# Kernel optimization log

Measured on AMD Instinct MI355X. Metric: run time of the kernel, lower is better.

Reference implementation:

```python
import jax, jax.numpy as jnp
import numpy as np

V, E, H, DV = 32000, 512, 1024, 512
B, K = 64, 49


def setup_inputs():
    key = jax.random.key(0)
    ks = jax.random.split(key, 16)
    p = lambda i, shape: jax.random.normal(ks[i], shape, dtype=jnp.float32) * 0.02
    return {
        "thought": jax.random.normal(ks[0], (B, H), dtype=jnp.float32),
        "visual_features": jax.random.normal(ks[1], (B, K, DV), dtype=jnp.float32),
        "max_len": 64,
        "embedding": p(2, (V, E)),
        "Wih1": p(3, (4 * H, E)), "Whh1": p(4, (4 * H, H)),
        "bih1": jnp.zeros((4 * H,), jnp.float32), "bhh1": jnp.zeros((4 * H,), jnp.float32),
        "Wih2": p(5, (4 * H, H)), "Whh2": p(6, (4 * H, H)),
        "bih2": jnp.zeros((4 * H,), jnp.float32), "bhh2": jnp.zeros((4 * H,), jnp.float32),
        "Wg1": p(7, (H, H)), "bg1": jnp.zeros((H,), jnp.float32),
        "Wg2": p(8, (1, H)), "bg2": jnp.zeros((1,), jnp.float32),
        "Wo": p(9, (V, H)), "bo": jnp.zeros((V,), jnp.float32),
        "Wv": p(10, (H, DV)), "bv": jnp.zeros((H,), jnp.float32),
        "ln_g": jnp.ones((H,), jnp.float32), "ln_b": jnp.zeros((H,), jnp.float32),
    }


def _lstm_cell(x, h, c, Wih, Whh, bih, bhh):
    # PyTorch LSTM gate order: i, f, g, o
    z = x @ Wih.T + h @ Whh.T + bih + bhh
    i, f, g, o = jnp.split(z, 4, axis=-1)
    c_new = jax.nn.sigmoid(f) * c + jax.nn.sigmoid(i) * jnp.tanh(g)
    h_new = jax.nn.sigmoid(o) * jnp.tanh(c_new)
    return h_new, c_new


def reference(thought, visual_features, max_len, embedding, Wih1, Whh1, bih1, bhh1,
              Wih2, Whh2, bih2, bbh2=None, bih2_dummy=None, **_unused):
    raise RuntimeError('placeholder')


def reference(thought, visual_features, max_len, embedding, Wih1, Whh1, bih1, bhh1,
              Wih2, Whh2, bih2, bhh2, Wg1, bg1, Wg2, bg2, Wo, bo, Wv, bv, ln_g, ln_b):
    Bsz, Hd = thought.shape
    temperature = 0.4  # epoch = 0 -> 0.4 + 0.4*0
    top_p = 0.7        # epoch = 0 -> 0.7 + 0.2*0
    scale = 1.0 / jnp.sqrt(jnp.asarray(Hd, jnp.float32))
    # visual_proj: Linear + LayerNorm (Dropout is identity in eval mode)
    vp = visual_features @ Wv.T + bv
    mu = vp.mean(-1, keepdims=True)
    var = vp.var(-1, keepdims=True)
    vp = (vp - mu) / jnp.sqrt(var + 1e-5) * ln_g + ln_b  # [B,K,H]
    b_idx = jnp.arange(Bsz)
    # carry: (h1,c1,h2,c2, input token, last-3 token history, history validity)
    init = (thought, jnp.zeros_like(thought), thought, jnp.zeros_like(thought),
            jnp.full((Bsz,), 1, jnp.int32),
            jnp.zeros((Bsz, 3), jnp.int32), jnp.zeros((Bsz, 3), jnp.bool_))
    keys = jax.random.split(jax.random.key(42), max_len)

    def step(carry, key):
        h1, c1, h2, c2, inp, hist, histv = carry
        emb = embedding[inp]  # [B,E]
        h1, c1 = _lstm_cell(emb, h1, c1, Wih1, Whh1, bih1, bhh1)
        h2, c2 = _lstm_cell(h1, h2, c2, Wih2, Whh2, bih2, bhh2)
        gate = jax.nn.sigmoid(jnp.tanh(h2 @ Wg1.T + bg1) @ Wg2.T + bg2)  # [B,1]
        out = h2 * gate
        attn = jax.nn.softmax(jnp.einsum('bh,bkh->bk', out, vp) * scale, axis=-1)
        out = out + jnp.einsum('bk,bkh->bh', attn, vp)
        logits = out @ Wo.T + bo  # [B,V]
        # repetition penalty: -2.0 once per UNIQUE token in last-3 history (set semantics via .max)
        pen = jnp.zeros_like(logits).at[b_idx[:, None], hist].max(histv.astype(logits.dtype))
        logits = (logits - 2.0 * pen) / temperature
        # nucleus (top-p) filtering, matching top_k_top_p_filtering with top_k=0
        order = jnp.argsort(-logits, axis=-1)
        sl = jnp.take_along_axis(logits, order, axis=-1)
        cum = jnp.cumsum(jax.nn.softmax(sl, axis=-1), axis=-1)
        rem = cum > top_p
        rem = jnp.concatenate([jnp.zeros_like(rem[:, :1]), rem[:, :-1]], axis=-1)
        mask = jnp.zeros_like(rem).at[b_idx[:, None], order].set(rem)
        logits = jnp.where(mask, -jnp.inf, logits)
        nxt = jax.random.categorical(key, logits).astype(jnp.int32)  # multinomial sample
        hist = jnp.concatenate([hist[:, 1:], nxt[:, None]], axis=1)
        histv = jnp.concatenate([histv[:, 1:], jnp.ones((Bsz, 1), jnp.bool_)], axis=1)
        return (h1, c1, h2, c2, nxt, hist, histv), nxt

    _, toks = jax.lax.scan(step, init, keys)
    return toks.T  # [B, max_len]
```

## Files before the change

### kernel.cpp

```cpp
#include <hip/hip_runtime.h>
#include <hip/hip_bf16.h>
#include <stdint.h>


#define B_   64
#define H_   1024
#define E_   512
#define DV_  512
#define KV_  49
#define V_   32000
#define T_   64

__device__ __forceinline__ uint32_t rotl32(uint32_t x, int r) {
  return (x << r) | (x >> (32 - r));
}
__device__ __forceinline__ void tf2x32(uint32_t k0, uint32_t k1,
                                       uint32_t x0, uint32_t x1,
                                       uint32_t& o0, uint32_t& o1) {
  uint32_t ks0 = k0, ks1 = k1, ks2 = k0 ^ k1 ^ 0x1BD11BDAu;
  x0 += ks0; x1 += ks1;
#define RND_(r) { x0 += x1; x1 = rotl32(x1, r) ^ x0; }
  RND_(13) RND_(15) RND_(26) RND_(6)  x0 += ks1; x1 += ks2 + 1u;
  RND_(17) RND_(29) RND_(16) RND_(24) x0 += ks2; x1 += ks0 + 2u;
  RND_(13) RND_(15) RND_(26) RND_(6)  x0 += ks0; x1 += ks1 + 3u;
  RND_(17) RND_(29) RND_(16) RND_(24) x0 += ks1; x1 += ks2 + 4u;
  RND_(13) RND_(15) RND_(26) RND_(6)  x0 += ks2; x1 += ks0 + 5u;
#undef RND_
  o0 = x0; o1 = x1;
}

__device__ __forceinline__ unsigned key_of(float f) {
  unsigned u = __float_as_uint(f);
  return (u & 0x80000000u) ? ~u : (u | 0x80000000u);
}
__device__ __forceinline__ float sigf(float x) { return 1.0f / (1.0f + expf(-x)); }

__global__ __launch_bounds__(256)
void gemm32(const float* __restrict__ A0, int lda0, const float* __restrict__ W0,
            int ldw0, int K0, float* __restrict__ out0, int ldo0, int nt0,
            const float* __restrict__ A1, int lda1, const float* __restrict__ W1,
            int ldw1, int K1, float* __restrict__ out1, int ldo1) {
  __shared__ __align__(16) float As[64][36];
  __shared__ __align__(16) float Ws[32][36];
  int tid = threadIdx.x;
  int bx = blockIdx.x;
  const float* A; const float* W; float* out;
  int lda, ldw, K, ldo, n0;
  if (bx < nt0) { A = A0; W = W0; out = out0; lda = lda0; ldw = ldw0; K = K0; ldo = ldo0; n0 = bx * 32; }
  else          { A = A1; W = W1; out = out1; lda = lda1; ldw = ldw1; K = K1; ldo = ldo1; n0 = (bx - nt0) * 32; }
  int m0 = blockIdx.y * 64;
  int tc = tid & 15, tr = tid >> 4;
  float acc[4][2] = {};
  for (int kc = 0; kc < K; kc += 32) {
#pragma unroll
    for (int l = tid; l < 768; l += 256) {
      if (l < 512) {
        int r = l >> 3, c4 = l & 7;
        *(float4*)&As[r][c4 * 4] =
            *(const float4*)&A[(long long)(m0 + r) * lda + kc + c4 * 4];
      } else {
        int q = l - 512;
        int r = q >> 3, c4 = q & 7;
        *(float4*)&Ws[r][c4 * 4] =
            *(const float4*)&W[(long long)(n0 + r) * ldw + kc + c4 * 4];
      }
    }
    __syncthreads();
#pragma unroll
    for (int kk4 = 0; kk4 < 8; kk4++) {
      float4 a4[4], w4[2];
#pragma unroll
      for (int i = 0; i < 4; i++) a4[i] = *(const float4*)&As[tr * 4 + i][kk4 * 4];
#pragma unroll
      for (int j = 0; j < 2; j++) w4[j] = *(const float4*)&Ws[tc * 2 + j][kk4 * 4];
#pragma unroll
      for (int i = 0; i < 4; i++)
#pragma unroll
        for (int j = 0; j < 2; j++) {
          acc[i][j] = fmaf(a4[i].x, w4[j].x, acc[i][j]);
          acc[i][j] = fmaf(a4[i].y, w4[j].y, acc[i][j]);
          acc[i][j] = fmaf(a4[i].z, w4[j].z, acc[i][j]);
          acc[i][j] = fmaf(a4[i].w, w4[j].w, acc[i][j]);
        }
    }
    __syncthreads();
  }
#pragma unroll
  for (int i = 0; i < 4; i++)
#pragma unroll
    for (int j = 0; j < 2; j++)
      out[(long long)(m0 + tr * 4 + i) * ldo + n0 + tc * 2 + j] = acc[i][j];
}

__global__ __launch_bounds__(256)
void ln_vp(float* __restrict__ vp, const float* __restrict__ bv,
           const float* __restrict__ g, const float* __restrict__ bt) {
  int row = blockIdx.x, tid = threadIdx.x;
  __shared__ float buf[H_];
  __shared__ float red[256];
  float* p = vp + (long long)row * H_;
  for (int h = tid; h < H_; h += 256) buf[h] = __fadd_rn(p[h], bv[h]);
  __syncthreads();
  float s = 0;
  for (int h = tid; h < H_; h += 256) s += buf[h];
  red[tid] = s; __syncthreads();
  for (int off = 128; off > 0; off >>= 1) { if (tid < off) red[tid] += red[tid + off]; __syncthreads(); }
  float mu = red[0] / (float)H_;
  __syncthreads();
  float vs = 0;
  for (int h = tid; h < H_; h += 256) { float d = buf[h] - mu; vs += d * d; }
  red[tid] = vs; __syncthreads();
  for (int off = 128; off > 0; off >>= 1) { if (tid < off) red[tid] += red[tid + off]; __syncthreads(); }
  float var = red[0] / (float)H_;
  float sq = sqrtf(var + 1e-5f);
  for (int h = tid; h < H_; h += 256) {
    float nrm = __fdiv_rn(__fsub_rn(buf[h], mu), sq);
    p[h] = __fadd_rn(__fmul_rn(nrm, g[h]), bt[h]);
  }
}

__global__ __launch_bounds__(256)
void lstm_cell2(const float* __restrict__ dx, const float* __restrict__ dh,
                const float* __restrict__ bih, const float* __restrict__ bhh,
                float* __restrict__ c,
                float* __restrict__ hA, int ldA, float* __restrict__ hB, int ldB) {
  int idx = blockIdx.x * 256 + threadIdx.x;
  int b = idx >> 10, h = idx & 1023;
  float z[4];
#pragma unroll
  for (int g = 0; g < 4; g++) {
    int j = g * 1024 + h;
    float s = __fadd_rn(dx[b * 4096 + j], dh[b * 4096 + j]);
    s = __fadd_rn(s, bih[j]);
    s = __fadd_rn(s, bhh[j]);
    z[g] = s;
  }
  float fc = __fmul_rn(sigf(z[1]), c[idx]);
  float ig = __fmul_rn(sigf(z[0]), tanhf(z[2]));
  float cn = __fadd_rn(fc, ig);
  float hn = __fmul_rn(sigf(z[3]), tanhf(cn));
  c[idx] = cn;
  hA[(long long)b * ldA + h] = hn;
  hB[(long long)b * ldB + h] = hn;
}

__global__ __launch_bounds__(256)
void gate_attn(const float* __restrict__ dg, const float* __restrict__ bg1,
               const float* __restrict__ Wg2, const float* __restrict__ bg2,
               const float* __restrict__ h2buf, const float* __restrict__ vp,
               float* __restrict__ ctx) {
  int b = blockIdx.x, tid = threadIdx.x;
  __shared__ float t1[H_], outv[H_], attn[64];
  __shared__ float gate_s;
  for (int h = tid; h < H_; h += 256)
    t1[h] = tanhf(__fadd_rn(dg[b * H_ + h], bg1[h]));
  __syncthreads();
  if (tid == 0) {
    float s = 0;
    for (int h = 0; h < H_; h++) s = fmaf(t1[h], Wg2[h], s);
    gate_s = sigf(__fadd_rn(s, bg2[0]));
  }
  __syncthreads();
  float gate = gate_s;
  for (int h = tid; h < H_; h += 256) outv[h] = __fmul_rn(h2buf[b * H_ + h], gate);
  __syncthreads();
  if (tid < KV_) {
    const float* vrow = vp + ((long long)b * KV_ + tid) * H_;
    float a = 0;
    for (int h = 0; h < H_; h++) a = fmaf(outv[h], vrow[h], a);
    attn[tid] = __fmul_rn(a, 0.03125f);
  }
  __syncthreads();
  if (tid == 0) {
    float m = -INFINITY;
    for (int k = 0; k < KV_; k++) m = fmaxf(m, attn[k]);
    float ss = 0;
    for (int k = 0; k < KV_; k++) { attn[k] = expf(attn[k] - m); ss += attn[k]; }
    for (int k = 0; k < KV_; k++) attn[k] = __fdiv_rn(attn[k], ss);
  }
  __syncthreads();
  for (int h = tid; h < H_; h += 256) {
    float acc = 0;
    for (int k = 0; k < KV_; k++) acc = fmaf(attn[k], vp[((long long)b * KV_ + k) * H_ + h], acc);
    ctx[b * H_ + h] = __fadd_rn(outv[h], acc);
  }
}

__global__ __launch_bounds__(256)
void init_state(const float* __restrict__ thought, const float* __restrict__ embedding,
                float* c1, float* c2, float* xcat1, float* xcat2,
                int* hist, int* histv) {
  int i = blockIdx.x * 256 + threadIdx.x;
  if (i < B_ * H_) {
    int b = i >> 10, h = i & 1023;
    c1[i] = 0.f; c2[i] = 0.f;
    float th = thought[i];
    xcat1[b * (E_ + H_) + E_ + h] = th;
    xcat2[b * (2 * H_) + H_ + h] = th;
    if (h < E_) xcat1[b * (E_ + H_) + h] = embedding[E_ + h];
  }
  if (i < B_ * 3) { hist[i] = 0; histv[i] = 0; }
}

__global__ __launch_bounds__(1024)
void sample_kernel(const float* __restrict__ dlog, const float* __restrict__ bo,
                   float* __restrict__ Lbuf, float* __restrict__ Ebuf,
                   int* __restrict__ hist, int* __restrict__ histv,
                   const float* __restrict__ embedding, float* __restrict__ xcat1,
                   int* __restrict__ outTok, int t) {
  int b = blockIdx.x, tid = threadIdx.x;
  __shared__ float redf[1024];
  __shared__ int   redi[1024];
  __shared__ unsigned long long binS[256], suf[256];
  __shared__ unsigned binC[256];
  __shared__ int jstar_s;
  __shared__ unsigned long long carry_s;
  __shared__ unsigned prefix_s;

  int hh0 = hist[b * 3 + 0], hh1 = hist[b * 3 + 1], hh2 = hist[b * 3 + 2];
  int p0 = histv[b * 3 + 0] ? hh0 : -1;
  int p1 = histv[b * 3 + 1] ? hh1 : -1;
  int p2 = histv[b * 3 + 2] ? hh2 : -1;
  const float* pa = dlog + (long long)b * V_;
  float* L = Lbuf + (long long)b * V_;
  float* E = Ebuf + (long long)b * V_;

  float lm = -INFINITY;
  for (int v = tid; v < V_; v += 1024) {
    float raw = __fadd_rn(pa[v], bo[v]);
    if (v == p0 || v == p1 || v == p2) raw = __fsub_rn(raw, 2.0f);
    float l = __fdiv_rn(raw, 0.4f);
    L[v] = l;
    lm = fmaxf(lm, l);
  }
  redf[tid] = lm; __syncthreads();
  for (int off = 512; off > 0; off >>= 1) { if (tid < off) redf[tid] = fmaxf(redf[tid], redf[tid + off]); __syncthreads(); }
  float m = redf[0];
  __syncthreads();

  float ls = 0;
  for (int v = tid; v < V_; v += 1024) { float e = expf(L[v] - m); E[v] = e; ls += e; }
  redf[tid] = ls; __syncthreads();
  for (int off = 512; off > 0; off >>= 1) { if (tid < off) redf[tid] += redf[tid + off]; __syncthreads(); }
  float Z = redf[0];
  __syncthreads();

  const double SC = 17592186044416.0;
  const unsigned long long B0 =
      (unsigned long long)(0.699999988079071044921875 * 17592186044416.0);
  if (tid == 0) { carry_s = 0ull; prefix_s = 0u; }
  __syncthreads();
  for (int pass = 0; pass < 4; pass++) {
    int shift = 24 - 8 * pass;
    unsigned maskk = (pass == 0) ? 0u : (0xFFFFFFFFu << (shift + 8));
    if (tid < 256) { binS[tid] = 0ull; binC[tid] = 0u; }
    __syncthreads();
    unsigned pref = prefix_s;
    unsigned long long carry = carry_s;
    for (int v = tid; v < V_; v += 1024) {
      unsigned key = key_of(L[v]);
      if ((key & maskk) == pref) {
        unsigned bin = (key >> shift) & 255u;
        unsigned long long S = (unsigned long long)((double)(E[v] / Z) * SC);
        atomicAdd(&binS[bin], S);
        atomicAdd(&binC[bin], 1u);
      }
    }
    __syncthreads();
    if (tid < 256) suf[tid] = binS[tid];
    __syncthreads();
    for (int off = 1; off < 256; off <<= 1) {
      unsigned long long add = 0ull;
      if (tid < 256 && tid + off < 256) add = suf[tid + off];
      __syncthreads();
      if (tid < 256) suf[tid] += add;
      __syncthreads();
    }
    if (tid == 0) jstar_s = 256;
    __syncthreads();
    if (tid < 256 && binC[tid] > 0u) {
      unsigned long long A = carry + ((tid < 255) ? suf[tid + 1] : 0ull);
      if (A <= B0) atomicMin(&jstar_s, tid);
    }
    __syncthreads();
    if (tid == 0) {
      int j = jstar_s;
      carry_s = carry + ((j < 255) ? suf[j + 1] : 0ull);
      prefix_s = pref | (((unsigned)j) << shift);
    }
    __syncthreads();
  }
  unsigned Kstar = prefix_s;

  unsigned kt0, kt1;
  tf2x32(0u, 42u, 0u, (unsigned)t, kt0, kt1);

  float bestv = -INFINITY; int besti = 0x7fffffff;
  for (int v = tid; v < V_; v += 1024) {
    float l = L[v];
    if (key_of(l) >= Kstar) {
      unsigned r0, r1;
      tf2x32(kt0, kt1, 0u, (unsigned)(b * V_ + v), r0, r1);
      unsigned bits = r0 ^ r1;
      float u = __uint_as_float((bits >> 9) | 0x3f800000u) - 1.0f;
      u = fmaxf(u, 1.17549435e-38f);
      float gum = -logf(-logf(u));
      float val = __fadd_rn(l, gum);
      if (val > bestv) { bestv = val; besti = v; }
    }
  }
  redf[tid] = bestv; redi[tid] = besti; __syncthreads();
  for (int off = 512; off > 0; off >>= 1) {
    if (tid < off) {
      float ov = redf[tid + off]; int oi = redi[tid + off];
      if (ov > redf[tid] || (ov == redf[tid] && oi < redi[tid])) { redf[tid] = ov; redi[tid] = oi; }
    }
    __syncthreads();
  }
  int tok = redi[0];
  if (tid == 0) {
    outTok[b * T_ + t] = tok;
    hist[b * 3 + 0] = hh1; hist[b * 3 + 1] = hh2; hist[b * 3 + 2] = tok;
    int v1 = histv[b * 3 + 1], v2 = histv[b * 3 + 2];
    histv[b * 3 + 0] = v1; histv[b * 3 + 1] = v2; histv[b * 3 + 2] = 1;
  }
  for (int k = tid; k < E_; k += 1024)
    xcat1[b * (E_ + H_) + k] = embedding[(long long)tok * E_ + k];
}

extern "C" void kernel_launch(void* const* d_in, const int* in_sizes, int n_in,
                              void* d_out, int out_size, void* d_ws, size_t ws_size,
                              hipStream_t stream) {
  const float* thought   = (const float*)d_in[0];
  const float* visf      = (const float*)d_in[1];
  const float* embedding = (const float*)d_in[3];
  const float* Wih1 = (const float*)d_in[4];
  const float* Whh1 = (const float*)d_in[5];
  const float* bih1 = (const float*)d_in[6];
  const float* bhh1 = (const float*)d_in[7];
  const float* Wih2 = (const float*)d_in[8];
  const float* Whh2 = (const float*)d_in[9];
  const float* bih2 = (const float*)d_in[10];
  const float* bhh2 = (const float*)d_in[11];
  const float* Wg1  = (const float*)d_in[12];
  const float* bg1  = (const float*)d_in[13];
  const float* Wg2  = (const float*)d_in[14];
  const float* bg2  = (const float*)d_in[15];
  const float* Wo   = (const float*)d_in[16];
  const float* bo   = (const float*)d_in[17];
  const float* Wv   = (const float*)d_in[18];
  const float* bv   = (const float*)d_in[19];
  const float* ln_g = (const float*)d_in[20];
  const float* ln_b = (const float*)d_in[21];
  int* outTok = (int*)d_out;

  float* ws = (float*)d_ws;
  long long off = 0;
  float* vp    = ws + off; off += (long long)B_ * KV_ * H_;
  float* xcat1 = ws + off; off += B_ * (E_ + H_);
  float* xcat2 = ws + off; off += B_ * (2 * H_);
  float* c1    = ws + off; off += B_ * H_;
  float* c2    = ws + off; off += B_ * H_;
  float* h2buf = ws + off; off += B_ * H_;
  float* ctx   = ws + off; off += B_ * H_;
  float* dx    = ws + off; off += (long long)B_ * 4096;
  float* dh    = ws + off; off += (long long)B_ * 4096;
  float* dg    = ws + off; off += (long long)B_ * H_;
  float* dlog  = ws + off; off += (long long)B_ * V_;
  float* Lbuf  = ws + off; off += (long long)B_ * V_;
  float* Ebuf  = ws + off; off += (long long)B_ * V_;
  int* hist  = (int*)(ws + off); off += 256;
  int* histv = (int*)(ws + off); off += 256;

  init_state<<<256, 256, 0, stream>>>(thought, embedding, c1, c2, xcat1, xcat2, hist, histv);

  gemm32<<<dim3(32, KV_), 256, 0, stream>>>(
      visf, DV_, Wv, DV_, DV_, vp, H_, 32,
      visf, DV_, Wv, DV_, DV_, vp, H_);
  ln_vp<<<B_ * KV_, 256, 0, stream>>>(vp, bv, ln_g, ln_b);

  for (int t = 0; t < T_; t++) {
    gemm32<<<dim3(256, 1), 256, 0, stream>>>(
        xcat1, E_ + H_, Wih1, E_, E_, dx, 4096, 128,
        xcat1 + E_, E_ + H_, Whh1, H_, H_, dh, 4096);
    lstm_cell2<<<256, 256, 0, stream>>>(dx, dh, bih1, bhh1, c1,
                                        xcat1 + E_, E_ + H_, xcat2, 2 * H_);
    gemm32<<<dim3(256, 1), 256, 0, stream>>>(
        xcat2, 2 * H_, Wih2, H_, H_, dx, 4096, 128,
        xcat2 + H_, 2 * H_, Whh2, H_, H_, dh, 4096);
    lstm_cell2<<<256, 256, 0, stream>>>(dx, dh, bih2, bhh2, c2,
                                        h2buf, H_, xcat2 + H_, 2 * H_);
    gemm32<<<dim3(32, 1), 256, 0, stream>>>(
        h2buf, H_, Wg1, H_, H_, dg, H_, 32,
        h2buf, H_, Wg1, H_, H_, dg, H_);
    gate_attn<<<B_, 256, 0, stream>>>(dg, bg1, Wg2, bg2, h2buf, vp, ctx);
    gemm32<<<dim3(1000, 1), 256, 0, stream>>>(
        ctx, H_, Wo, H_, H_, dlog, V_, 1000,
        ctx, H_, Wo, H_, H_, dlog, V_);
    sample_kernel<<<B_, 1024, 0, stream>>>(dlog, bo, Lbuf, Ebuf, hist, histv,
                                           embedding, xcat1, outTok, t);
  }
}
```

Before: 31.90 ms.

## Register-prefetch GEMM tiles, add 64x64 GEMM, keep sampling data in registers

The gemm32 kernel now uses a K-tile of 64 and prefetches the next tile's global loads into registers while computing the current one. A new gemm64 kernel with 64x64 output tiles replaces gemm32 for the visual projection and the vocabulary projection, so each thread reuses its shared-memory loads across more outputs. The sampling kernel keeps its per-thread logits and probabilities in register arrays instead of global scratch buffers, and replaces the shared-memory suffix scan with a wavefront shuffle scan plus ballot. In exchange, register pressure rises, which may lower occupancy, and the 1024-thread sampling kernel carries 64 floats per thread that could spill.

Result: slower. 85.14 ms (+166.9%).

```diff
diff --git a/kernel.cpp b/kernel.cpp
--- a/kernel.cpp
+++ b/kernel.cpp
@@ -40,8 +40,8 @@
             int ldw0, int K0, float* __restrict__ out0, int ldo0, int nt0,
             const float* __restrict__ A1, int lda1, const float* __restrict__ W1,
             int ldw1, int K1, float* __restrict__ out1, int ldo1) {
-  __shared__ __align__(16) float As[64][36];
-  __shared__ __align__(16) float Ws[32][36];
+  __shared__ __align__(16) float As[64][68];
+  __shared__ __align__(16) float Ws[32][68];
   int tid = threadIdx.x;
   int bx = blockIdx.x;
   const float* A; const float* W; float* out;
@@ -50,24 +50,35 @@
   else          { A = A1; W = W1; out = out1; lda = lda1; ldw = ldw1; K = K1; ldo = ldo1; n0 = (bx - nt0) * 32; }
   int m0 = blockIdx.y * 64;
   int tc = tid & 15, tr = tid >> 4;
+  int ar[4], ac[4], wr[2], wc[2];
+#pragma unroll
+  for (int s = 0; s < 4; s++) { int l = tid + s * 256; ar[s] = l >> 4; ac[s] = (l & 15) * 4; }
+#pragma unroll
+  for (int s = 0; s < 2; s++) { int l = tid + s * 256; wr[s] = l >> 4; wc[s] = (l & 15) * 4; }
+  float4 pa[4], pw[2];
+#pragma unroll
+  for (int s = 0; s < 4; s++)
+    pa[s] = *(const float4*)&A[(long long)(m0 + ar[s]) * lda + ac[s]];
+#pragma unroll
+  for (int s = 0; s < 2; s++)
+    pw[s] = *(const float4*)&W[(long long)(n0 + wr[s]) * ldw + wc[s]];
   float acc[4][2] = {};
-  for (int kc = 0; kc < K; kc += 32) {
-#pragma unroll
-    for (int l = tid; l < 768; l += 256) {
-      if (l < 512) {
-        int r = l >> 3, c4 = l & 7;
-        *(float4*)&As[r][c4 * 4] =
-            *(const float4*)&A[(long long)(m0 + r) * lda + kc + c4 * 4];
-      } else {
-        int q = l - 512;
-        int r = q >> 3, c4 = q & 7;
-        *(float4*)&Ws[r][c4 * 4] =
-            *(const float4*)&W[(long long)(n0 + r) * ldw + kc + c4 * 4];
-      }
-    }
-    __syncthreads();
-#pragma unroll
-    for (int kk4 = 0; kk4 < 8; kk4++) {
+  for (int kc = 0; kc < K; kc += 64) {
+#pragma unroll
+    for (int s = 0; s < 4; s++) *(float4*)&As[ar[s]][ac[s]] = pa[s];
+#pragma unroll
+    for (int s = 0; s < 2; s++) *(float4*)&Ws[wr[s]][wc[s]] = pw[s];
+    __syncthreads();
+    if (kc + 64 < K) {
+#pragma unroll
+      for (int s = 0; s < 4; s++)
+        pa[s] = *(const float4*)&A[(long long)(m0 + ar[s]) * lda + kc + 64 + ac[s]];
+#pragma unroll
+      for (int s = 0; s < 2; s++)
+        pw[s] = *(const float4*)&W[(long long)(n0 + wr[s]) * ldw + kc + 64 + wc[s]];
+    }
+#pragma unroll
+    for (int kk4 = 0; kk4 < 16; kk4++) {
       float4 a4[4], w4[2];
 #pragma unroll
       for (int i = 0; i < 4; i++) a4[i] = *(const float4*)&As[tr * 4 + i][kk4 * 4];
@@ -90,6 +101,65 @@
 #pragma unroll
     for (int j = 0; j < 2; j++)
       out[(long long)(m0 + tr * 4 + i) * ldo + n0 + tc * 2 + j] = acc[i][j];
+}
+
+__global__ __launch_bounds__(256)
+void gemm64(const float* __restrict__ A, int lda,
+            const float* __restrict__ W, int ldw, int K,
+            float* __restrict__ out, int ldo) {
+  __shared__ __align__(16) float As[64][68];
+  __shared__ __align__(16) float Ws[64][68];
+  int tid = threadIdx.x;
+  int n0 = blockIdx.x * 64, m0 = blockIdx.y * 64;
+  int tc = tid & 15, tr = tid >> 4;
+  int r4[4], c4[4];
+#pragma unroll
+  for (int s = 0; s < 4; s++) { int l = tid + s * 256; r4[s] = l >> 4; c4[s] = (l & 15) * 4; }
+  float4 pa[4], pw[4];
+#pragma unroll
+  for (int s = 0; s < 4; s++) {
+    pa[s] = *(const float4*)&A[(long long)(m0 + r4[s]) * lda + c4[s]];
+    pw[s] = *(const float4*)&W[(long long)(n0 + r4[s]) * ldw + c4[s]];
+  }
+  float acc[4][4] = {};
+  for (int kc = 0; kc < K; kc += 64) {
+#pragma unroll
+    for (int s = 0; s < 4; s++) {
+      *(float4*)&As[r4[s]][c4[s]] = pa[s];
+      *(float4*)&Ws[r4[s]][c4[s]] = pw[s];
+    }
+    __syncthreads();
+    if (kc + 64 < K) {
+#pragma unroll
+      for (int s = 0; s < 4; s++) {
+        pa[s] = *(const float4*)&A[(long long)(m0 + r4[s]) * lda + kc + 64 + c4[s]];
+        pw[s] = *(const float4*)&W[(long long)(n0 + r4[s]) * ldw + kc + 64 + c4[s]];
+      }
+    }
+#pragma unroll
+    for (int kk4 = 0; kk4 < 16; kk4++) {
+      float4 a4[4], w4[4];
+#pragma unroll
+      for (int i = 0; i < 4; i++) a4[i] = *(const float4*)&As[tr * 4 + i][kk4 * 4];
+#pragma unroll
+      for (int j = 0; j < 4; j++) w4[j] = *(const float4*)&Ws[tc * 4 + j][kk4 * 4];
+#pragma unroll
+      for (int i = 0; i < 4; i++)
+#pragma unroll
+        for (int j = 0; j < 4; j++) {
+          acc[i][j] = fmaf(a4[i].x, w4[j].x, acc[i][j]);
+          acc[i][j] = fmaf(a4[i].y, w4[j].y, acc[i][j]);
+          acc[i][j] = fmaf(a4[i].z, w4[j].z, acc[i][j]);
+          acc[i][j] = fmaf(a4[i].w, w4[j].w, acc[i][j]);
+        }
+    }
+    __syncthreads();
+  }
+#pragma unroll
+  for (int i = 0; i < 4; i++)
+#pragma unroll
+    for (int j = 0; j < 4; j++)
+      out[(long long)(m0 + tr * 4 + i) * ldo + n0 + tc * 4 + j] = acc[i][j];
 }
 
 __global__ __launch_bounds__(256)
@@ -204,34 +274,35 @@
 
 __global__ __launch_bounds__(1024)
 void sample_kernel(const float* __restrict__ dlog, const float* __restrict__ bo,
-                   float* __restrict__ Lbuf, float* __restrict__ Ebuf,
                    int* __restrict__ hist, int* __restrict__ histv,
                    const float* __restrict__ embedding, float* __restrict__ xcat1,
                    int* __restrict__ outTok, int t) {
   int b = blockIdx.x, tid = threadIdx.x;
   __shared__ float redf[1024];
   __shared__ int   redi[1024];
-  __shared__ unsigned long long binS[256], suf[256];
+  __shared__ unsigned long long binS[256];
   __shared__ unsigned binC[256];
-  __shared__ int jstar_s;
   __shared__ unsigned long long carry_s;
   __shared__ unsigned prefix_s;
 
-  int hh0 = hist[b * 3 + 0], hh1 = hist[b * 3 + 1], hh2 = hist[b * 3 + 2];
-  int p0 = histv[b * 3 + 0] ? hh0 : -1;
+  int hh1 = hist[b * 3 + 1], hh2 = hist[b * 3 + 2];
+  int p0 = histv[b * 3 + 0] ? hist[b * 3 + 0] : -1;
   int p1 = histv[b * 3 + 1] ? hh1 : -1;
   int p2 = histv[b * 3 + 2] ? hh2 : -1;
   const float* pa = dlog + (long long)b * V_;
-  float* L = Lbuf + (long long)b * V_;
-  float* E = Ebuf + (long long)b * V_;
-
+
+  float Lr[32], q[32];
   float lm = -INFINITY;
-  for (int v = tid; v < V_; v += 1024) {
-    float raw = __fadd_rn(pa[v], bo[v]);
-    if (v == p0 || v == p1 || v == p2) raw = __fsub_rn(raw, 2.0f);
-    float l = __fdiv_rn(raw, 0.4f);
-    L[v] = l;
-    lm = fmaxf(lm, l);
+#pragma unroll
+  for (int i = 0; i < 32; i++) {
+    int v = i * 1024 + tid;
+    if (i < 31 || tid < 256) {
+      float raw = __fadd_rn(pa[v], bo[v]);
+      if (v == p0 || v == p1 || v == p2) raw = __fsub_rn(raw, 2.0f);
+      float l = __fdiv_rn(raw, 0.4f);
+      Lr[i] = l;
+      lm = fmaxf(lm, l);
+    } else Lr[i] = -INFINITY;
   }
   redf[tid] = lm; __syncthreads();
   for (int off = 512; off > 0; off >>= 1) { if (tid < off) redf[tid] = fmaxf(redf[tid], redf[tid + off]); __syncthreads(); }
@@ -239,17 +310,24 @@
   __syncthreads();
 
   float ls = 0;
-  for (int v = tid; v < V_; v += 1024) { float e = expf(L[v] - m); E[v] = e; ls += e; }
+#pragma unroll
+  for (int i = 0; i < 32; i++) {
+    if (i < 31 || tid < 256) { float e = expf(Lr[i] - m); q[i] = e; ls += e; }
+    else q[i] = 0.f;
+  }
   redf[tid] = ls; __syncthreads();
   for (int off = 512; off > 0; off >>= 1) { if (tid < off) redf[tid] += redf[tid + off]; __syncthreads(); }
   float Z = redf[0];
   __syncthreads();
+#pragma unroll
+  for (int i = 0; i < 32; i++)
+    if (i < 31 || tid < 256) q[i] = __fdiv_rn(q[i], Z);
 
   const double SC = 17592186044416.0;
   const unsigned long long B0 =
       (unsigned long long)(0.699999988079071044921875 * 17592186044416.0);
   if (tid == 0) { carry_s = 0ull; prefix_s = 0u; }
-  __syncthreads();
+#pragma unroll
   for (int pass = 0; pass < 4; pass++) {
     int shift = 24 - 8 * pass;
     unsigned maskk = (pass == 0) ? 0u : (0xFFFFFFFFu << (shift + 8));
@@ -257,36 +335,47 @@
     __syncthreads();
     unsigned pref = prefix_s;
     unsigned long long carry = carry_s;
-    for (int v = tid; v < V_; v += 1024) {
-      unsigned key = key_of(L[v]);
-      if ((key & maskk) == pref) {
-        unsigned bin = (key >> shift) & 255u;
-        unsigned long long S = (unsigned long long)((double)(E[v] / Z) * SC);
-        atomicAdd(&binS[bin], S);
-        atomicAdd(&binC[bin], 1u);
+#pragma unroll
+    for (int i = 0; i < 32; i++) {
+      if (i < 31 || tid < 256) {
+        unsigned key = key_of(Lr[i]);
+        if ((key & maskk) == pref) {
+          unsigned bin = (key >> shift) & 255u;
+          unsigned long long S = (unsigned long long)((double)q[i] * SC);
+          atomicAdd(&binS[bin], S);
+          atomicAdd(&binC[bin], 1u);
+        }
       }
     }
     __syncthreads();
-    if (tid < 256) suf[tid] = binS[tid];
-    __syncthreads();
-    for (int off = 1; off < 256; off <<= 1) {
-      unsigned long long add = 0ull;
-      if (tid < 256 && tid + off < 256) add = suf[tid + off];
-      __syncthreads();
-      if (tid < 256) suf[tid] += add;
-      __syncthreads();
-    }
-    if (tid == 0) jstar_s = 256;
-    __syncthreads();
-    if (tid < 256 && binC[tid] > 0u) {
-      unsigned long long A = carry + ((tid < 255) ? suf[tid + 1] : 0ull);
-      if (A <= B0) atomicMin(&jstar_s, tid);
-    }
-    __syncthreads();
-    if (tid == 0) {
-      int j = jstar_s;
-      carry_s = carry + ((j < 255) ? suf[j + 1] : 0ull);
-      prefix_s = pref | (((unsigned)j) << shift);
+    if (tid < 64) {
+      unsigned long long b0 = binS[4 * tid + 0], b1 = binS[4 * tid + 1];
+      unsigned long long b2 = binS[4 * tid + 2], b3 = binS[4 * tid + 3];
+      unsigned c0 = binC[4 * tid + 0], c1 = binC[4 * tid + 1];
+      unsigned c2 = binC[4 * tid + 2], c3 = binC[4 * tid + 3];
+      unsigned long long s3 = b3, s2 = b2 + s3, s1 = b1 + s2, s0 = b0 + s1;
+      unsigned long long SUF = s0;
+#pragma unroll
+      for (int off = 1; off < 64; off <<= 1) {
+        unsigned long long tsh = __shfl_down((unsigned long long)SUF, off, 64);
+        SUF += (tid + off < 64) ? tsh : 0ull;
+      }
+      unsigned long long Snext = __shfl_down((unsigned long long)SUF, 1, 64);
+      if (tid == 63) Snext = 0ull;
+      unsigned long long a0 = s1 + Snext, a1 = s2 + Snext, a2 = s3 + Snext, a3 = Snext;
+      int localj = 256; unsigned long long mysuf = 0ull;
+      if (c0 > 0u && carry + a0 <= B0)                  { localj = 4 * tid + 0; mysuf = a0; }
+      else if (c1 > 0u && carry + a1 <= B0)             { localj = 4 * tid + 1; mysuf = a1; }
+      else if (c2 > 0u && carry + a2 <= B0)             { localj = 4 * tid + 2; mysuf = a2; }
+      else if (c3 > 0u && carry + a3 <= B0)             { localj = 4 * tid + 3; mysuf = a3; }
+      unsigned long long ball = __ballot(localj != 256);
+      int firstlane = __ffsll((long long)ball) - 1;
+      int j = __shfl(localj, firstlane, 64);
+      unsigned long long sj = __shfl((unsigned long long)mysuf, firstlane, 64);
+      if (tid == 0) {
+        carry_s = carry + sj;
+        prefix_s = pref | (((unsigned)j) << shift);
+      }
     }
     __syncthreads();
   }
@@ -296,17 +385,21 @@
   tf2x32(0u, 42u, 0u, (unsigned)t, kt0, kt1);
 
   float bestv = -INFINITY; int besti = 0x7fffffff;
-  for (int v = tid; v < V_; v += 1024) {
-    float l = L[v];
-    if (key_of(l) >= Kstar) {
-      unsigned r0, r1;
-      tf2x32(kt0, kt1, 0u, (unsigned)(b * V_ + v), r0, r1);
-      unsigned bits = r0 ^ r1;
-      float u = __uint_as_float((bits >> 9) | 0x3f800000u) - 1.0f;
-      u = fmaxf(u, 1.17549435e-38f);
-      float gum = -logf(-logf(u));
-      float val = __fadd_rn(l, gum);
-      if (val > bestv) { bestv = val; besti = v; }
+#pragma unroll
+  for (int i = 0; i < 32; i++) {
+    if (i < 31 || tid < 256) {
+      int v = i * 1024 + tid;
+      float l = Lr[i];
+      if (key_of(l) >= Kstar) {
+        unsigned r0, r1;
+        tf2x32(kt0, kt1, 0u, (unsigned)(b * V_ + v), r0, r1);
+        unsigned bits = r0 ^ r1;
+        float u = __uint_as_float((bits >> 9) | 0x3f800000u) - 1.0f;
+        u = fmaxf(u, 1.17549435e-38f);
+        float gum = -logf(-logf(u));
+        float val = __fadd_rn(l, gum);
+        if (val > bestv) { bestv = val; besti = v; }
+      }
     }
   }
   redf[tid] = bestv; redi[tid] = besti; __syncthreads();
@@ -367,16 +460,12 @@
   float* dh    = ws + off; off += (long long)B_ * 4096;
   float* dg    = ws + off; off += (long long)B_ * H_;
   float* dlog  = ws + off; off += (long long)B_ * V_;
-  float* Lbuf  = ws + off; off += (long long)B_ * V_;
-  float* Ebuf  = ws + off; off += (long long)B_ * V_;
   int* hist  = (int*)(ws + off); off += 256;
   int* histv = (int*)(ws + off); off += 256;
 
   init_state<<<256, 256, 0, stream>>>(thought, embedding, c1, c2, xcat1, xcat2, hist, histv);
 
-  gemm32<<<dim3(32, KV_), 256, 0, stream>>>(
-      visf, DV_, Wv, DV_, DV_, vp, H_, 32,
-      visf, DV_, Wv, DV_, DV_, vp, H_);
+  gemm64<<<dim3(16, KV_), 256, 0, stream>>>(visf, DV_, Wv, DV_, DV_, vp, H_);
   ln_vp<<<B_ * KV_, 256, 0, stream>>>(vp, bv, ln_g, ln_b);
 
   for (int t = 0; t < T_; t++) {
@@ -394,10 +483,8 @@
         h2buf, H_, Wg1, H_, H_, dg, H_, 32,
         h2buf, H_, Wg1, H_, H_, dg, H_);
     gate_attn<<<B_, 256, 0, stream>>>(dg, bg1, Wg2, bg2, h2buf, vp, ctx);
-    gemm32<<<dim3(1000, 1), 256, 0, stream>>>(
-        ctx, H_, Wo, H_, H_, dlog, V_, 1000,
-        ctx, H_, Wo, H_, H_, dlog, V_);
-    sample_kernel<<<B_, 1024, 0, stream>>>(dlog, bo, Lbuf, Ebuf, hist, histv,
+    gemm64<<<dim3(500, 1), 256, 0, stream>>>(ctx, H_, Wo, H_, H_, dlog, V_);
+    sample_kernel<<<B_, 1024, 0, stream>>>(dlog, bo, hist, histv,
                                            embedding, xcat1, outTok, t);
   }
 }
```
